# Kernel optimization log

Hardware: AMD Instinct MI355X
Metric: run time of the kernel (lower is better)

Reference implementation:

```python
import jax, jax.numpy as jnp
import numpy as np

HIDDEN = 1024
NUM_HEADS = 16
HEAD_DIM = HIDDEN // NUM_HEADS
BATCH = 2
SEQ = 2048


def setup_inputs() -> dict:
    key = jax.random.key(0)
    k1, k2, k3 = jax.random.split(key, 3)
    hidden_states = jax.random.normal(k1, (BATCH, SEQ, HIDDEN), dtype=jnp.float32)
    attention_mask = jnp.zeros((BATCH, 1, SEQ, SEQ), dtype=jnp.float32)
    # nn.Linear weights: stored as [out_features, in_features]
    w_qkv = jax.random.normal(k2, (3 * HIDDEN, HIDDEN), dtype=jnp.float32) * (HIDDEN ** -0.5)
    w_o = jax.random.normal(k3, (HIDDEN, HIDDEN), dtype=jnp.float32) * (HIDDEN ** -0.5)
    return {"hidden_states": hidden_states, "attention_mask": attention_mask,
            "w_qkv": w_qkv, "w_o": w_o}


def reference(hidden_states, attention_mask, w_qkv, w_o):
    B, S, H = hidden_states.shape
    scale = HEAD_DIM ** -0.5
    qkv = jnp.einsum('bsh,oh->bso', hidden_states, w_qkv)  # [B,S,3H]
    qkv = qkv.reshape(B, S, 3, NUM_HEADS, HEAD_DIM)
    q = qkv[:, :, 0].transpose(0, 2, 1, 3)  # [B,nH,S,hd]
    k = qkv[:, :, 1].transpose(0, 2, 1, 3)
    v = qkv[:, :, 2].transpose(0, 2, 1, 3)
    attn = jnp.einsum('bhqd,bhkd->bhqk', q, k) * scale
    attn = attn + attention_mask
    attn = jax.nn.softmax(attn, axis=-1)
    out = jnp.einsum('bhqk,bhkd->bhqd', attn, v)
    out = out.transpose(0, 2, 1, 3).reshape(B, S, H)
    return jnp.einsum('bsh,oh->bso', out, w_o)
```

## Files before the change

kernel.cpp:

```cpp
#include <hip/hip_runtime.h>

typedef unsigned short u16;
using bf16x8 = __attribute__((ext_vector_type(8))) __bf16;
using f32x4  = __attribute__((ext_vector_type(4))) float;
using u16x8  = __attribute__((ext_vector_type(8))) unsigned short;
using u16x4  = __attribute__((ext_vector_type(4))) unsigned short;

#define SEQ   2048
#define HID   1024
#define NHEAD 16
#define HD    64
#define BATCH 2
#define NTOK  4096

__device__ __forceinline__ u16 f2bf(float f) {
  unsigned u = __builtin_bit_cast(unsigned, f);
  u += 0x7fffu + ((u >> 16) & 1u);
  return (u16)(u >> 16);
}

__device__ __forceinline__ void gld_lds16(const void* g, void* l) {
  __builtin_amdgcn_global_load_lds(
      (__attribute__((address_space(1))) void*)(__UINTPTR_TYPE__)g,
      (__attribute__((address_space(3))) void*)l, 16, 0, 0);
}

__device__ __forceinline__ unsigned cvtpk(float lo, float hi) {
  unsigned r;
  asm("v_cvt_pk_bf16_f32 %0, %1, %2" : "=v"(r) : "v"(lo), "v"(hi));
  return r;
}

template<int CTRL>
__device__ __forceinline__ float row_ror(float x) {
  int xi = __builtin_bit_cast(int, x);
  int r  = __builtin_amdgcn_update_dpp(xi, xi, CTRL, 0xf, 0xf, false);
  return __builtin_bit_cast(float, r);
}
__device__ __forceinline__ float rowmax16(float x) {
  x = fmaxf(x, row_ror<0x121>(x));
  x = fmaxf(x, row_ror<0x122>(x));
  x = fmaxf(x, row_ror<0x124>(x));
  x = fmaxf(x, row_ror<0x128>(x));
  return x;
}
__device__ __forceinline__ float rowsum16(float x) {
  x += row_ror<0x121>(x);
  x += row_ror<0x122>(x);
  x += row_ror<0x124>(x);
  x += row_ror<0x128>(x);
  return x;
}

__global__ __launch_bounds__(256) void cvt3_kernel(const float* __restrict__ a, u16* __restrict__ oa,
                                                   const float* __restrict__ b, u16* __restrict__ ob,
                                                   const float* __restrict__ c, u16* __restrict__ oc) {
  const float* in; u16* out; int off;
  int bid = blockIdx.x;
  if (bid < 4096)      { in = a; out = oa; off = bid; }
  else if (bid < 7168) { in = b; out = ob; off = bid - 4096; }
  else                 { in = c; out = oc; off = bid - 7168; }
  int i = (off * 256 + threadIdx.x) * 4;
  float4 v = *reinterpret_cast<const float4*>(in + i);
  u16x4 o = { f2bf(v.x), f2bf(v.y), f2bf(v.z), f2bf(v.w) };
  *reinterpret_cast<u16x4*>(out + i) = o;
}

template<bool BF16OUT>
__global__ __launch_bounds__(256) void gemm_bt(const u16* __restrict__ A,
                                               const u16* __restrict__ B,
                                               void* __restrict__ Cv,
                                               int M, int N, int K) {
  __shared__ u16 At[128 * 64];
  __shared__ u16 Bt[128 * 64];
  const int tid  = threadIdx.x;
  const int wave = tid >> 6;
  const int lane = tid & 63;
  const int g    = lane >> 4;
  const int r16  = lane & 15;
  const int wr   = wave >> 1;
  const int wc   = wave & 1;
  const int bm   = blockIdx.y;
  const int bn   = blockIdx.x;

  const u16* Ab = A + (size_t)bm * 128 * K;
  const u16* Bb = B + (size_t)bn * 128 * K;
  const int srow = lane >> 3;
  const int scol = (lane & 7) * 8;

  f32x4 acc[4][4] = {};

  for (int kt = 0; kt < K; kt += 64) {
#pragma unroll
    for (int c = 0; c < 4; ++c) {
      int seg = wave * 4 + c;
      gld_lds16(Ab + (size_t)(seg * 8 + srow) * K + kt + scol, &At[seg * 512]);
      gld_lds16(Bb + (size_t)(seg * 8 + srow) * K + kt + scol, &Bt[seg * 512]);
    }
    __syncthreads();
#pragma unroll
    for (int ko = 0; ko < 64; ko += 32) {
      bf16x8 af[4], bfr[4];
#pragma unroll
      for (int mi = 0; mi < 4; ++mi)
        af[mi] = *reinterpret_cast<const bf16x8*>(&At[(wr * 64 + mi * 16 + r16) * 64 + ko + g * 8]);
#pragma unroll
      for (int ni = 0; ni < 4; ++ni)
        bfr[ni] = *reinterpret_cast<const bf16x8*>(&Bt[(wc * 64 + ni * 16 + r16) * 64 + ko + g * 8]);
#pragma unroll
      for (int mi = 0; mi < 4; ++mi)
#pragma unroll
        for (int ni = 0; ni < 4; ++ni)
          acc[mi][ni] = __builtin_amdgcn_mfma_f32_16x16x32_bf16(af[mi], bfr[ni], acc[mi][ni], 0, 0, 0);
    }
    __syncthreads();
  }

#pragma unroll
  for (int mi = 0; mi < 4; ++mi)
#pragma unroll
    for (int ni = 0; ni < 4; ++ni) {
      int row0 = bm * 128 + wr * 64 + mi * 16 + g * 4;
      int col  = bn * 128 + wc * 64 + ni * 16 + r16;
#pragma unroll
      for (int r = 0; r < 4; ++r) {
        float v = acc[mi][ni][r];
        if (BF16OUT) ((u16*)Cv)[(size_t)(row0 + r) * N + col] = f2bf(v);
        else         ((float*)Cv)[(size_t)(row0 + r) * N + col] = v;
      }
    }
}

__global__ __launch_bounds__(256) void gemm_bt64(const u16* __restrict__ A,
                                                 const u16* __restrict__ B,
                                                 float* __restrict__ C,
                                                 int M, int N, int K) {
  __shared__ u16 At[128 * 64];
  __shared__ u16 Bt[64 * 64];
  const int tid  = threadIdx.x;
  const int wave = tid >> 6;
  const int lane = tid & 63;
  const int g    = lane >> 4;
  const int r16  = lane & 15;
  const int bm   = blockIdx.y;
  const int bn   = blockIdx.x;

  const u16* Ab = A + (size_t)bm * 128 * K;
  const u16* Bb = B + (size_t)bn * 64 * K;
  const int srow = lane >> 3;
  const int scol = (lane & 7) * 8;

  f32x4 acc[2][4] = {};

  for (int kt = 0; kt < K; kt += 64) {
#pragma unroll
    for (int c = 0; c < 4; ++c) {
      int seg = wave * 4 + c;
      gld_lds16(Ab + (size_t)(seg * 8 + srow) * K + kt + scol, &At[seg * 512]);
    }
#pragma unroll
    for (int c = 0; c < 2; ++c) {
      int seg = wave * 2 + c;
      gld_lds16(Bb + (size_t)(seg * 8 + srow) * K + kt + scol, &Bt[seg * 512]);
    }
    __syncthreads();
#pragma unroll
    for (int ko = 0; ko < 64; ko += 32) {
      bf16x8 af[2], bfr[4];
#pragma unroll
      for (int mi = 0; mi < 2; ++mi)
        af[mi] = *reinterpret_cast<const bf16x8*>(&At[(wave * 32 + mi * 16 + r16) * 64 + ko + g * 8]);
#pragma unroll
      for (int ni = 0; ni < 4; ++ni)
        bfr[ni] = *reinterpret_cast<const bf16x8*>(&Bt[(ni * 16 + r16) * 64 + ko + g * 8]);
#pragma unroll
      for (int mi = 0; mi < 2; ++mi)
#pragma unroll
        for (int ni = 0; ni < 4; ++ni)
          acc[mi][ni] = __builtin_amdgcn_mfma_f32_16x16x32_bf16(af[mi], bfr[ni], acc[mi][ni], 0, 0, 0);
    }
    __syncthreads();
  }

#pragma unroll
  for (int mi = 0; mi < 2; ++mi)
#pragma unroll
    for (int ni = 0; ni < 4; ++ni) {
      int row0 = bm * 128 + wave * 32 + mi * 16 + g * 4;
      int col  = bn * 64 + ni * 16 + r16;
#pragma unroll
      for (int r = 0; r < 4; ++r)
        C[(size_t)(row0 + r) * N + col] = acc[mi][ni][r];
    }
}

__global__ __launch_bounds__(256, 4) void attn_kernel(const u16* __restrict__ qkv,
                                                      const float* __restrict__ mask,
                                                      u16* __restrict__ AO) {
  __shared__ u16 Kt[2][64 * 64];
  __shared__ u16 Vt[64 * 64];
  __shared__ u16 Pl[4][16 * 64];

  const int tid  = threadIdx.x;
  const int w    = tid >> 6;
  const int lane = tid & 63;
  const int g    = lane >> 4;
  const int r16  = lane & 15;

  const int n  = blockIdx.x;
  const int x  = n & 7;
  const int s_ = n >> 3;
  const int h  = s_ & 15;
  const int t_ = ((s_ >> 4) << 3) + x;
  const int b  = t_ >> 5;
  const int qt = t_ & 31;

  const size_t tokbase = (size_t)b * SEQ;

  bf16x8 aq[2];
  {
    int qrow = qt * 64 + w * 16 + r16;
#pragma unroll
    for (int ko = 0; ko < 2; ++ko)
      aq[ko] = *reinterpret_cast<const bf16x8*>(
          qkv + ((tokbase + qrow) * 3 + 0) * HID + h * HD + ko * 32 + g * 8);
  }

  f32x4 o[4] = {};
  float mrow[4], lrow[4];
#pragma unroll
  for (int r = 0; r < 4; ++r) { mrow[r] = -3.0e38f; lrow[r] = 0.f; }

  const int srowK = lane >> 3;
  const int vkey  = tid >> 2;
  const int vd3   = tid & 3;

#define STAGE_K(buf, kb)                                                        \
  {                                                                             \
    _Pragma("unroll")                                                           \
    for (int c = 0; c < 2; ++c) {                                               \
      int seg = w * 2 + c;                                                      \
      int sK  = ((seg >> 1) + srowK) & 7;                                       \
      int srcc = (lane & 7) ^ sK;                                               \
      gld_lds16(qkv + ((tokbase + (kb) + seg * 8 + srowK) * 3 + 1) * HID +      \
                    h * HD + srcc * 8,                                          \
                &Kt[buf][seg * 512]);                                           \
    }                                                                           \
  }

  STAGE_K(0, 0);

#pragma unroll 1
  for (int kb = 0; kb < SEQ; kb += 64) {
    const int cur = (kb >> 6) & 1;
    const int nxt = cur ^ 1;
    const bool more = (kb + 64) < SEQ;

    float mpre[4][4];
#pragma unroll
    for (int r = 0; r < 4; ++r) {
      int q = qt * 64 + w * 16 + g * 4 + r;
      const float* mp = mask + ((size_t)b * SEQ + q) * SEQ + kb;
#pragma unroll
      for (int ni = 0; ni < 4; ++ni) mpre[r][ni] = mp[ni * 16 + r16];
    }
    const u16* vp = qkv + ((tokbase + kb + vkey) * 3 + 2) * HID + h * HD + vd3 * 16;
    u16x8 v0 = *reinterpret_cast<const u16x8*>(vp);
    u16x8 v1 = *reinterpret_cast<const u16x8*>(vp + 8);

    __syncthreads();

#pragma unroll
    for (int j = 0; j < 16; ++j) {
      u16 val = (j < 8) ? (u16)v0[j] : (u16)v1[j - 8];
      int row = vd3 * 16 + j;
      int sV  = (vd3 + (j & 7)) & 7;
      Vt[row * 64 + (((vkey >> 3) ^ sV) << 3) + (vkey & 7)] = val;
    }
    __syncthreads();

    f32x4 sf[4] = {};
    __builtin_amdgcn_s_setprio(1);
#pragma unroll
    for (int ko = 0; ko < 2; ++ko) {
      bf16x8 bk[4];
#pragma unroll
      for (int ni = 0; ni < 4; ++ni) {
        int row = ni * 16 + r16;
        int sK  = (ni + (r16 & 7)) & 7;
        bk[ni] = *reinterpret_cast<const bf16x8*>(
            &Kt[cur][row * 64 + (((ko * 4 + g) ^ sK) << 3)]);
      }
#pragma unroll
      for (int ni = 0; ni < 4; ++ni)
        sf[ni] = __builtin_amdgcn_mfma_f32_16x16x32_bf16(aq[ko], bk[ni], sf[ni], 0, 0, 0);
    }
    __builtin_amdgcn_s_setprio(0);

    float mx[4];
#pragma unroll
    for (int r = 0; r < 4; ++r) {
      float m_ = -3.0e38f;
#pragma unroll
      for (int ni = 0; ni < 4; ++ni) {
        float sv = sf[ni][r] * 0.125f + mpre[r][ni];
        sf[ni][r] = sv;
        m_ = fmaxf(m_, sv);
      }
      mx[r] = rowmax16(m_);
    }
    float need = 0.f;
#pragma unroll
    for (int r = 0; r < 4; ++r) need = fmaxf(need, mx[r] - mrow[r]);
    if (__any(need > 8.0f)) {
#pragma unroll
      for (int r = 0; r < 4; ++r) {
        float mnew  = fmaxf(mrow[r], mx[r]);
        float alpha = __expf(mrow[r] - mnew);
        mrow[r] = mnew;
        lrow[r] *= alpha;
#pragma unroll
        for (int di = 0; di < 4; ++di) o[di][r] *= alpha;
      }
    }
#pragma unroll
    for (int r = 0; r < 4; ++r) {
      float p0 = __expf(sf[0][r] - mrow[r]);
      float p1 = __expf(sf[1][r] - mrow[r]);
      float p2 = __expf(sf[2][r] - mrow[r]);
      float p3 = __expf(sf[3][r] - mrow[r]);
      float s  = rowsum16(p0 + p1 + p2 + p3);
      lrow[r] += s;
      unsigned pk01 = cvtpk(p0, p1);
      unsigned pk23 = cvtpk(p2, p3);
      int prow = g * 4 + r;
      int sP   = prow & 7;
      u16 pv[4] = { (u16)pk01, (u16)(pk01 >> 16), (u16)pk23, (u16)(pk23 >> 16) };
#pragma unroll
      for (int ni = 0; ni < 4; ++ni) {
        int chunk = ni * 2 + (r16 >> 3);
        Pl[w][prow * 64 + ((chunk ^ sP) << 3) + (r16 & 7)] = pv[ni];
      }
    }

    if (more) STAGE_K(nxt, kb + 64);

    __builtin_amdgcn_s_setprio(1);
#pragma unroll
    for (int kk = 0; kk < 2; ++kk) {
      bf16x8 pa, bv[4];
      pa = *reinterpret_cast<const bf16x8*>(
          &Pl[w][r16 * 64 + (((kk * 4 + g) ^ (r16 & 7)) << 3)]);
#pragma unroll
      for (int di = 0; di < 4; ++di) {
        int row = di * 16 + r16;
        int sV  = (di + (r16 & 7)) & 7;
        bv[di] = *reinterpret_cast<const bf16x8*>(
            &Vt[row * 64 + (((kk * 4 + g) ^ sV) << 3)]);
      }
#pragma unroll
      for (int di = 0; di < 4; ++di)
        o[di] = __builtin_amdgcn_mfma_f32_16x16x32_bf16(pa, bv[di], o[di], 0, 0, 0);
    }
    __builtin_amdgcn_s_setprio(0);
  }

#pragma unroll
  for (int di = 0; di < 4; ++di)
#pragma unroll
    for (int r = 0; r < 4; ++r) {
      int srow = qt * 64 + w * 16 + g * 4 + r;
      float val = o[di][r] / lrow[r];
      AO[(tokbase + srow) * HID + h * HD + di * 16 + r16] = f2bf(val);
    }
#undef STAGE_K
}

extern "C" void kernel_launch(void* const* d_in, const int* in_sizes, int n_in,
                              void* d_out, int out_size, void* d_ws, size_t ws_size,
                              hipStream_t stream) {
  (void)in_sizes; (void)n_in; (void)out_size; (void)ws_size;
  const float* hs   = (const float*)d_in[0];
  const float* mask = (const float*)d_in[1];
  const float* wqkv = (const float*)d_in[2];
  const float* wo   = (const float*)d_in[3];
  float* out = (float*)d_out;

  char* ws   = (char*)d_ws;
  u16* Xb    = (u16*)(ws);
  u16* Wqkvb = (u16*)(ws + 8u  * 1024 * 1024);
  u16* Wob   = (u16*)(ws + 14u * 1024 * 1024);
  u16* QKVb  = (u16*)(ws + 16u * 1024 * 1024);
  u16* AOb   = (u16*)(ws + 40u * 1024 * 1024);

  cvt3_kernel<<<8192, 256, 0, stream>>>(hs, Xb, wqkv, Wqkvb, wo, Wob);

  gemm_bt<true><<<dim3(3072 / 128, 4096 / 128), 256, 0, stream>>>(Xb, Wqkvb, QKVb, NTOK, 3072, HID);
  attn_kernel  <<<1024, 256, 0, stream>>>(QKVb, mask, AOb);
  gemm_bt64    <<<dim3(1024 / 64, 4096 / 128), 256, 0, stream>>>(AOb, Wob, out, NTOK, 1024, HID);
}
```

Before: 174.9 us.

## Pre-transpose V in a separate kernel and double-buffer async V staging

Adds a kernel that transposes V from the QKV buffer into a per-(batch,head) [HD][SEQ] layout in workspace. The attention kernel then stages V tiles with direct global-to-LDS async loads into a double buffer, prefetched alongside K. This removes the per-iteration scalar transposing LDS stores and one barrier from the attention inner loop. In exchange it adds an extra kernel launch, about 8 MB of extra memory traffic and 8 KB more LDS per block, which could lower occupancy.

```diff
diff --git a/kernel.cpp b/kernel.cpp
--- a/kernel.cpp
+++ b/kernel.cpp
@@ -64,6 +64,38 @@
   float4 v = *reinterpret_cast<const float4*>(in + i);
   u16x4 o = { f2bf(v.x), f2bf(v.y), f2bf(v.z), f2bf(v.w) };
   *reinterpret_cast<u16x4*>(out + i) = o;
+}
+
+__global__ __launch_bounds__(256) void vtrans_kernel(const u16* __restrict__ qkv,
+                                                     u16* __restrict__ VT) {
+  __shared__ u16 Ls[64][80];
+  const int tid = threadIdx.x;
+  const int kt  = blockIdx.x;
+  const int bh  = blockIdx.y;
+  const int b   = bh >> 4, h = bh & 15;
+  const int key0 = kt * 64;
+  {
+    int r  = tid >> 2;
+    int d0 = (tid & 3) * 16;
+    const u16* src = qkv + (((size_t)b * SEQ + key0 + r) * 3 + 2) * HID + h * HD + d0;
+    u16x8 a = *reinterpret_cast<const u16x8*>(src);
+    u16x8 c = *reinterpret_cast<const u16x8*>(src + 8);
+    *reinterpret_cast<u16x8*>(&Ls[r][d0])     = a;
+    *reinterpret_cast<u16x8*>(&Ls[r][d0 + 8]) = c;
+  }
+  __syncthreads();
+  {
+    int d  = tid >> 2;
+    int k0 = (tid & 3) * 16;
+    u16x8 o0, o1;
+#pragma unroll
+    for (int j = 0; j < 8; ++j) o0[j] = Ls[k0 + j][d];
+#pragma unroll
+    for (int j = 0; j < 8; ++j) o1[j] = Ls[k0 + 8 + j][d];
+    u16* dst = VT + ((size_t)bh * HD + d) * SEQ + key0 + k0;
+    *reinterpret_cast<u16x8*>(dst)     = o0;
+    *reinterpret_cast<u16x8*>(dst + 8) = o1;
+  }
 }
 
 template<bool BF16OUT>
@@ -195,10 +227,11 @@
 }
 
 __global__ __launch_bounds__(256, 4) void attn_kernel(const u16* __restrict__ qkv,
+                                                      const u16* __restrict__ VT,
                                                       const float* __restrict__ mask,
                                                       u16* __restrict__ AO) {
   __shared__ u16 Kt[2][64 * 64];
-  __shared__ u16 Vt[64 * 64];
+  __shared__ u16 Vt[2][64 * 64];
   __shared__ u16 Pl[4][16 * 64];
 
   const int tid  = threadIdx.x;
@@ -216,6 +249,7 @@
   const int qt = t_ & 31;
 
   const size_t tokbase = (size_t)b * SEQ;
+  const u16* VTbh = VT + (size_t)(b * NHEAD + h) * HD * SEQ;
 
   bf16x8 aq[2];
   {
@@ -232,8 +266,6 @@
   for (int r = 0; r < 4; ++r) { mrow[r] = -3.0e38f; lrow[r] = 0.f; }
 
   const int srowK = lane >> 3;
-  const int vkey  = tid >> 2;
-  const int vd3   = tid & 3;
 
 #define STAGE_K(buf, kb)                                                        \
   {                                                                             \
@@ -247,8 +279,20 @@
                 &Kt[buf][seg * 512]);                                           \
     }                                                                           \
   }
+#define STAGE_V(buf, kb)                                                        \
+  {                                                                             \
+    _Pragma("unroll")                                                           \
+    for (int c = 0; c < 2; ++c) {                                               \
+      int seg = w * 2 + c;                                                      \
+      int sV  = ((seg >> 1) + srowK) & 7;                                       \
+      int srcc = (lane & 7) ^ sV;                                               \
+      gld_lds16(VTbh + (size_t)(seg * 8 + srowK) * SEQ + (kb) + srcc * 8,       \
+                &Vt[buf][seg * 512]);                                           \
+    }                                                                           \
+  }
 
   STAGE_K(0, 0);
+  STAGE_V(0, 0);
 
 #pragma unroll 1
   for (int kb = 0; kb < SEQ; kb += 64) {
@@ -264,19 +308,7 @@
 #pragma unroll
       for (int ni = 0; ni < 4; ++ni) mpre[r][ni] = mp[ni * 16 + r16];
     }
-    const u16* vp = qkv + ((tokbase + kb + vkey) * 3 + 2) * HID + h * HD + vd3 * 16;
-    u16x8 v0 = *reinterpret_cast<const u16x8*>(vp);
-    u16x8 v1 = *reinterpret_cast<const u16x8*>(vp + 8);
-
-    __syncthreads();
-
-#pragma unroll
-    for (int j = 0; j < 16; ++j) {
-      u16 val = (j < 8) ? (u16)v0[j] : (u16)v1[j - 8];
-      int row = vd3 * 16 + j;
-      int sV  = (vd3 + (j & 7)) & 7;
-      Vt[row * 64 + (((vkey >> 3) ^ sV) << 3) + (vkey & 7)] = val;
-    }
+
     __syncthreads();
 
     f32x4 sf[4] = {};
@@ -343,7 +375,7 @@
       }
     }
 
-    if (more) STAGE_K(nxt, kb + 64);
+    if (more) { STAGE_K(nxt, kb + 64); STAGE_V(nxt, kb + 64); }
 
     __builtin_amdgcn_s_setprio(1);
 #pragma unroll
@@ -356,7 +388,7 @@
         int row = di * 16 + r16;
         int sV  = (di + (r16 & 7)) & 7;
         bv[di] = *reinterpret_cast<const bf16x8*>(
-            &Vt[row * 64 + (((kk * 4 + g) ^ sV) << 3)]);
+            &Vt[cur][row * 64 + (((kk * 4 + g) ^ sV) << 3)]);
       }
 #pragma unroll
       for (int di = 0; di < 4; ++di)
@@ -374,6 +406,7 @@
       AO[(tokbase + srow) * HID + h * HD + di * 16 + r16] = f2bf(val);
     }
 #undef STAGE_K
+#undef STAGE_V
 }
 
 extern "C" void kernel_launch(void* const* d_in, const int* in_sizes, int n_in,
@@ -392,10 +425,12 @@
   u16* Wob   = (u16*)(ws + 14u * 1024 * 1024);
   u16* QKVb  = (u16*)(ws + 16u * 1024 * 1024);
   u16* AOb   = (u16*)(ws + 40u * 1024 * 1024);
+  u16* VT    = (u16*)(ws + 48u * 1024 * 1024);
 
   cvt3_kernel<<<8192, 256, 0, stream>>>(hs, Xb, wqkv, Wqkvb, wo, Wob);
 
   gemm_bt<true><<<dim3(3072 / 128, 4096 / 128), 256, 0, stream>>>(Xb, Wqkvb, QKVb, NTOK, 3072, HID);
-  attn_kernel  <<<1024, 256, 0, stream>>>(QKVb, mask, AOb);
+  vtrans_kernel<<<dim3(SEQ / 64, BATCH * NHEAD), 256, 0, stream>>>(QKVb, VT);
+  attn_kernel  <<<1024, 256, 0, stream>>>(QKVb, VT, mask, AOb);
   gemm_bt64    <<<dim3(1024 / 64, 4096 / 128), 256, 0, stream>>>(AOb, Wob, out, NTOK, 1024, HID);
 }
```

New measurement: 175.8 us. No clear change (+0.5%).
